# Optimization experiments

Hardware: AMD Instinct MI355X
Metric: run time of the kernel (lower is better)

## Reference

```python
import jax, jax.numpy as jnp
import numpy as np

EMB = 1024
HEADS = 16
HEAD_DIM = EMB // HEADS
FF = 4 * EMB
EPS = 1e-5


def setup_inputs() -> dict:
    key = jax.random.key(0)
    ks = jax.random.split(key, 16)
    s = 0.02
    return {
        "x": jax.random.normal(ks[0], (2, 2048, EMB), dtype=jnp.float32),
        "ln1_g": jnp.ones((EMB,), jnp.float32),
        "ln1_b": jnp.zeros((EMB,), jnp.float32),
        "Wq": jax.random.normal(ks[1], (EMB, EMB), jnp.float32) * s,
        "bq": jnp.zeros((EMB,), jnp.float32),
        "Wk": jax.random.normal(ks[2], (EMB, EMB), jnp.float32) * s,
        "bk": jnp.zeros((EMB,), jnp.float32),
        "Wv": jax.random.normal(ks[3], (EMB, EMB), jnp.float32) * s,
        "bv": jnp.zeros((EMB,), jnp.float32),
        "Wo": jax.random.normal(ks[4], (EMB, EMB), jnp.float32) * s,
        "bo": jnp.zeros((EMB,), jnp.float32),
        "ln2_g": jnp.ones((EMB,), jnp.float32),
        "ln2_b": jnp.zeros((EMB,), jnp.float32),
        "W1": jax.random.normal(ks[5], (EMB, FF), jnp.float32) * s,
        "b1": jnp.zeros((FF,), jnp.float32),
        "W2": jax.random.normal(ks[6], (FF, EMB), jnp.float32) * s,
        "b2": jnp.zeros((EMB,), jnp.float32),
    }


def _layernorm(x, g, b):
    mu = jnp.mean(x, axis=-1, keepdims=True)
    var = jnp.var(x, axis=-1, keepdims=True)
    return (x - mu) * jax.lax.rsqrt(var + EPS) * g + b


def _attention(x, Wq, bq, Wk, bk, Wv, bv, Wo, bo):
    B, T, C = x.shape
    # [B,T,C] -> [B,H,T,Dh]
    def split(y):
        return y.reshape(B, T, HEADS, HEAD_DIM).transpose(0, 2, 1, 3)
    Q = split(x @ Wq + bq)
    K = split(x @ Wk + bk)
    V = split(x @ Wv + bv)
    att = jnp.einsum("bhqd,bhkd->bhqk", Q, K) / np.sqrt(HEAD_DIM).astype(np.float32)
    causal = jnp.tril(jnp.ones((T, T), bool))
    att = jnp.where(causal, att, -jnp.inf)
    att = jax.nn.softmax(att, axis=-1)
    out = jnp.einsum("bhqk,bhkd->bhqd", att, V)
    out = out.transpose(0, 2, 1, 3).reshape(B, T, C)
    return out @ Wo + bo


def reference(x, ln1_g, ln1_b, Wq, bq, Wk, bk, Wv, bv, Wo, bo,
              ln2_g, ln2_b, W1, b1, W2, b2):
    # dropout is identity in eval mode
    x = x + _attention(_layernorm(x, ln1_g, ln1_b), Wq, bq, Wk, bk, Wv, bv, Wo, bo)
    h = _layernorm(x, ln2_g, ln2_b)
    h = jax.nn.gelu(h @ W1 + b1, approximate=False) @ W2 + b2
    return x + h
```

## Files before the change

kernel.cpp:

```cpp
#include <hip/hip_runtime.h>
#include <hip/hip_bf16.h>

typedef __attribute__((ext_vector_type(4))) float f32x4;
typedef __attribute__((ext_vector_type(8))) short bf16x8;
typedef unsigned int u32;
typedef unsigned short u16;

#define GASP __attribute__((address_space(1)))
#define LASP __attribute__((address_space(3)))

__device__ __forceinline__ u16 f2bf(float f) {
  u32 u = __float_as_uint(f);
  return (u16)((u + 0x7fffu + ((u >> 16) & 1u)) >> 16);
}

__device__ __forceinline__ u32 cvtpk(float lo, float hi) {
  u32 r;
  asm("v_cvt_pk_bf16_f32 %0, %1, %2" : "=v"(r) : "v"(lo), "v"(hi));
  return r;
}

__device__ __forceinline__ void gl_lds16(const void* g, void* l) {
  __builtin_amdgcn_global_load_lds((const GASP u32*)g, (LASP u32*)l, 16, 0, 0);
}

struct CastArgs {
  const float* s[6];
  u16* d[6];
};

__global__ __launch_bounds__(256) void cast_w(CastArgs a) {
  int bid = blockIdx.x;
  int w, t, K, N, kshift;
  if (bid < 4096)      { w = bid >> 10; t = bid & 1023; K = 1024; N = 1024; kshift = 5; }
  else if (bid < 8192) { w = 4; t = bid - 4096; K = 1024; N = 4096; kshift = 5; }
  else                 { w = 5; t = bid - 8192; K = 4096; N = 1024; kshift = 7; }
  int tk = t & ((1 << kshift) - 1);
  int tn = t >> kshift;
  int k0 = tk << 5, n0 = tn << 5;
  const float* src = a.s[w];
  u16* dst = a.d[w];
  __shared__ u16 tile[32][36];
  int r = threadIdx.x >> 3, c0 = (threadIdx.x & 7) << 2;
  float4 v = *(const float4*)&src[(size_t)(k0 + r) * N + n0 + c0];
  tile[c0 + 0][r] = f2bf(v.x);
  tile[c0 + 1][r] = f2bf(v.y);
  tile[c0 + 2][r] = f2bf(v.z);
  tile[c0 + 3][r] = f2bf(v.w);
  __syncthreads();
  ushort4 o;
  o.x = tile[r][c0 + 0];
  o.y = tile[r][c0 + 1];
  o.z = tile[r][c0 + 2];
  o.w = tile[r][c0 + 3];
  *(ushort4*)&dst[(size_t)(n0 + r) * K + k0 + c0] = o;
}

__global__ __launch_bounds__(256) void ln_k(const float* __restrict__ x, const float* __restrict__ g,
                                            const float* __restrict__ b, u16* __restrict__ out) {
  int row = blockIdx.x;
  int tid = threadIdx.x;
  float4 v = *(const float4*)&x[(size_t)row * 1024 + tid * 4];
  float s = v.x + v.y + v.z + v.w;
  float ss = v.x * v.x + v.y * v.y + v.z * v.z + v.w * v.w;
#pragma unroll
  for (int o = 32; o >= 1; o >>= 1) {
    s += __shfl_xor(s, o, 64);
    ss += __shfl_xor(ss, o, 64);
  }
  __shared__ float red[8];
  int wv = tid >> 6;
  if ((tid & 63) == 0) { red[wv] = s; red[wv + 4] = ss; }
  __syncthreads();
  s = red[0] + red[1] + red[2] + red[3];
  ss = red[4] + red[5] + red[6] + red[7];
  float mu = s * (1.0f / 1024.0f);
  float var = ss * (1.0f / 1024.0f) - mu * mu;
  float rstd = rsqrtf(var + 1e-5f);
  float4 gv = *(const float4*)&g[tid * 4];
  float4 bv = *(const float4*)&b[tid * 4];
  ushort4 o4;
  o4.x = f2bf((v.x - mu) * rstd * gv.x + bv.x);
  o4.y = f2bf((v.y - mu) * rstd * gv.y + bv.y);
  o4.z = f2bf((v.z - mu) * rstd * gv.z + bv.z);
  o4.w = f2bf((v.w - mu) * rstd * gv.w + bv.w);
  *(ushort4*)&out[(size_t)row * 1024 + tid * 4] = o4;
}

template <int MODE>
__global__ __launch_bounds__(512, 2) void gemm_256(
    const u16* __restrict__ A, const u16* __restrict__ Bt,
    const float* __restrict__ bias0, const float* __restrict__ bias1, const float* __restrict__ bias2,
    void* outp, int rm, int rn, int xn, int M, int N, int K) {
  __shared__ __align__(16) u16 As[4][128 * 64];
  __shared__ __align__(16) u16 Bs[4][128 * 64];
  char* asB = (char*)As;
  char* bsB = (char*)Bs;
  const int tid = threadIdx.x;
  const int w = tid >> 6, lane = tid & 63;
  const int xcd = blockIdx.x & 7, idx = blockIdx.x >> 3;
  const int mt = (xcd / xn) * rm + (idx % rm);
  const int nt = (xcd % xn) * rn + (idx / rm);
  const int m0 = mt << 8, n0 = nt << 8;

  const int rA = tid >> 3;
  const int csw = ((tid & 7) ^ (rA & 7)) * 8;
  const u16* pA = A + (size_t)(m0 + rA) * K + csw;
  const u16* pB = Bt + (size_t)(n0 + rA) * K + csw;
  const int dstOff = tid * 16;

#define STG_A(kt, h, d_) do {                                            \
    const u16* s_ = pA + (size_t)((h) * 128) * K + (size_t)(kt) * 64;    \
    char* l_ = asB + ((d_) * 2 + (h)) * 16384 + dstOff;                  \
    gl_lds16(s_, l_);                                                    \
    gl_lds16(s_ + (size_t)64 * K, l_ + 8192);                            \
  } while (0)
#define STG_B(kt, h, d_) do {                                            \
    const u16* s_ = pB + (size_t)((h) * 128) * K + (size_t)(kt) * 64;    \
    char* l_ = bsB + ((d_) * 2 + (h)) * 16384 + dstOff;                  \
    gl_lds16(s_, l_);                                                    \
    gl_lds16(s_ + (size_t)64 * K, l_ + 8192);                            \
  } while (0)

  const int wr = w >> 2, wc = w & 3;
  const int g = lane >> 4, qi = lane & 15;

  int aOff[8][2], bOff[4][2];
#pragma unroll
  for (int mm = 0; mm < 8; ++mm) {
    int row = mm * 16 + qi;
#pragma unroll
    for (int ks = 0; ks < 2; ++ks)
      aOff[mm][ks] = row * 128 + (((ks * 4 + g) ^ (qi & 7)) << 4);
  }
#pragma unroll
  for (int nn = 0; nn < 4; ++nn) {
    int rowb = (wc & 1) * 64 + nn * 16 + qi;
#pragma unroll
    for (int ks = 0; ks < 2; ++ks)
      bOff[nn][ks] = rowb * 128 + (((ks * 4 + g) ^ (qi & 7)) << 4);
  }

  f32x4 acc[8][4];
#pragma unroll
  for (int i = 0; i < 8; ++i)
#pragma unroll
    for (int j = 0; j < 4; ++j) acc[i][j] = f32x4{0.f, 0.f, 0.f, 0.f};

#define MFMA16(MB, A00, A01, A10, A11) do {                                              \
    __builtin_amdgcn_s_setprio(1);                                                       \
    acc[(MB)][0] = __builtin_amdgcn_mfma_f32_16x16x32_bf16(A00, bv[0][0], acc[(MB)][0], 0, 0, 0); \
    acc[(MB)][1] = __builtin_amdgcn_mfma_f32_16x16x32_bf16(A00, bv[1][0], acc[(MB)][1], 0, 0, 0); \
    acc[(MB)][2] = __builtin_amdgcn_mfma_f32_16x16x32_bf16(A00, bv[2][0], acc[(MB)][2], 0, 0, 0); \
    acc[(MB)][3] = __builtin_amdgcn_mfma_f32_16x16x32_bf16(A00, bv[3][0], acc[(MB)][3], 0, 0, 0); \
    acc[(MB) + 1][0] = __builtin_amdgcn_mfma_f32_16x16x32_bf16(A10, bv[0][0], acc[(MB) + 1][0], 0, 0, 0); \
    acc[(MB) + 1][1] = __builtin_amdgcn_mfma_f32_16x16x32_bf16(A10, bv[1][0], acc[(MB) + 1][1], 0, 0, 0); \
    acc[(MB) + 1][2] = __builtin_amdgcn_mfma_f32_16x16x32_bf16(A10, bv[2][0], acc[(MB) + 1][2], 0, 0, 0); \
    acc[(MB) + 1][3] = __builtin_amdgcn_mfma_f32_16x16x32_bf16(A10, bv[3][0], acc[(MB) + 1][3], 0, 0, 0); \
    acc[(MB)][0] = __builtin_amdgcn_mfma_f32_16x16x32_bf16(A01, bv[0][1], acc[(MB)][0], 0, 0, 0); \
    acc[(MB)][1] = __builtin_amdgcn_mfma_f32_16x16x32_bf16(A01, bv[1][1], acc[(MB)][1], 0, 0, 0); \
    acc[(MB)][2] = __builtin_amdgcn_mfma_f32_16x16x32_bf16(A01, bv[2][1], acc[(MB)][2], 0, 0, 0); \
    acc[(MB)][3] = __builtin_amdgcn_mfma_f32_16x16x32_bf16(A01, bv[3][1], acc[(MB)][3], 0, 0, 0); \
    acc[(MB) + 1][0] = __builtin_amdgcn_mfma_f32_16x16x32_bf16(A11, bv[0][1], acc[(MB) + 1][0], 0, 0, 0); \
    acc[(MB) + 1][1] = __builtin_amdgcn_mfma_f32_16x16x32_bf16(A11, bv[1][1], acc[(MB) + 1][1], 0, 0, 0); \
    acc[(MB) + 1][2] = __builtin_amdgcn_mfma_f32_16x16x32_bf16(A11, bv[2][1], acc[(MB) + 1][2], 0, 0, 0); \
    acc[(MB) + 1][3] = __builtin_amdgcn_mfma_f32_16x16x32_bf16(A11, bv[3][1], acc[(MB) + 1][3], 0, 0, 0); \
    __builtin_amdgcn_s_setprio(0);                                                       \
  } while (0)

#define RDA(dst0, dst1, MB)                                          \
    bf16x8 dst0##0 = *(const bf16x8*)(asB + aTB + aOff[(MB)][0]);     \
    bf16x8 dst0##1 = *(const bf16x8*)(asB + aTB + aOff[(MB)][1]);     \
    bf16x8 dst1##0 = *(const bf16x8*)(asB + aTB + aOff[(MB) + 1][0]); \
    bf16x8 dst1##1 = *(const bf16x8*)(asB + aTB + aOff[(MB) + 1][1]);

  const int T = K >> 6;
  STG_A(0, 0, 0); STG_A(0, 1, 0);
  STG_B(0, 0, 0); STG_B(0, 1, 0);
  asm volatile("s_waitcnt vmcnt(0)" ::: "memory");
  __builtin_amdgcn_s_barrier();

  for (int t = 0; t < T; ++t) {
    const int d = t & 1;
    const int aTB = (d * 2 + wr) * 16384;
    const int bTB = (d * 2 + (wc >> 1)) * 16384;
    bf16x8 bv[4][2];
#pragma unroll
    for (int nn = 0; nn < 4; ++nn) {
      bv[nn][0] = *(const bf16x8*)(bsB + bTB + bOff[nn][0]);
      bv[nn][1] = *(const bf16x8*)(bsB + bTB + bOff[nn][1]);
    }
    RDA(p0a, p0b, 0);
    if (t + 1 < T) STG_A(t + 1, 0, d ^ 1);
    MFMA16(0, p0a0, p0a1, p0b0, p0b1);
    RDA(p1a, p1b, 2);
    if (t + 1 < T) STG_A(t + 1, 1, d ^ 1);
    MFMA16(2, p1a0, p1a1, p1b0, p1b1);
    RDA(p2a, p2b, 4);
    if (t + 1 < T) STG_B(t + 1, 0, d ^ 1);
    MFMA16(4, p2a0, p2a1, p2b0, p2b1);
    RDA(p3a, p3b, 6);
    if (t + 1 < T) STG_B(t + 1, 1, d ^ 1);
    MFMA16(6, p3a0, p3a1, p3b0, p3b1);
    asm volatile("" ::: "memory");
    if (t + 1 < T) { asm volatile("s_waitcnt vmcnt(0)" ::: "memory"); }
    __builtin_amdgcn_s_barrier();
  }
#undef MFMA16
#undef RDA
#undef STG_A
#undef STG_B

  const int ci = lane & 15;
#pragma unroll
  for (int mm = 0; mm < 8; ++mm) {
#pragma unroll
    for (int nn = 0; nn < 4; ++nn) {
      int colb = n0 + wc * 64 + nn * 16 + ci;
      int rowbase = m0 + wr * 128 + mm * 16 + 4 * g;
      f32x4 c = acc[mm][nn];
      if constexpr (MODE == 2) {
        int sel = colb >> 10;
        int cc = colb & 1023;
        const float* bp = sel == 0 ? bias0 : (sel == 1 ? bias1 : bias2);
        float bb = bp[cc];
        int h = cc >> 6, dd = cc & 63;
        int b_ = rowbase >> 11, tt = rowbase & 2047;
        if (sel == 2) {
          u16* op = (u16*)outp + 2ull * (4096ull * 1024ull);
          ushort4 o4;
          o4.x = f2bf(c[0] + bb);
          o4.y = f2bf(c[1] + bb);
          o4.z = f2bf(c[2] + bb);
          o4.w = f2bf(c[3] + bb);
          *(ushort4*)&op[((size_t)(b_ * 16 + h) * 64 + dd) * 2048 + tt] = o4;
        } else {
          float scale = (sel == 0) ? 0.125f : 1.0f;
          u16* op = (u16*)outp + (size_t)sel * (4096ull * 1024ull);
#pragma unroll
          for (int r = 0; r < 4; ++r)
            op[((size_t)(b_ * 16 + h) * 2048 + tt + r) * 64 + dd] = f2bf((c[r] + bb) * scale);
        }
      } else {
        float bb = bias0[colb];
#pragma unroll
        for (int r = 0; r < 4; ++r) {
          float v = c[r] + bb;
          float gl = 0.5f * v * (1.0f + erff(v * 0.70710678118654752f));
          ((u16*)outp)[(size_t)(rowbase + r) * N + colb] = f2bf(gl);
        }
      }
    }
  }
}

__global__ __launch_bounds__(512) void gemm_sk(
    const u16* __restrict__ A, const u16* __restrict__ Bt,
    const float* __restrict__ bias0, float* __restrict__ outp,
    const float* __restrict__ res, int M, int N, int K) {
  __shared__ __align__(16) union SM {
    struct { u16 As[2][4][128 * 32]; u16 Bs[2][4][128 * 32]; } t;
    float red[16][4][4][64];
  } sm;
  const int tid = threadIdx.x;
  const int w8 = tid >> 6, lane = tid & 63;
  const int gg = w8 >> 2, wl = w8 & 3;
  const int m0 = blockIdx.y << 7, n0 = blockIdx.x << 7;

  char* asB = (char*)sm.t.As[gg];
  char* bsB = (char*)sm.t.Bs[gg];
  const u16* aS[2];
  const u16* bS[2];
#pragma unroll
  for (int i = 0; i < 2; ++i) {
    int p = wl * 2048 + i * 1024 + lane * 16;
    int r = p >> 6;
    int cl = ((p >> 4) & 3) ^ ((r >> 1) & 3);
    aS[i] = A + (size_t)(m0 + r) * K + gg * 32 + cl * 8;
    bS[i] = Bt + (size_t)(n0 + r) * K + gg * 32 + cl * 8;
  }
  f32x4 acc[4][4];
#pragma unroll
  for (int i = 0; i < 4; ++i)
#pragma unroll
    for (int j = 0; j < 4; ++j) acc[i][j] = f32x4{0.f, 0.f, 0.f, 0.f};

  const int wr = wl >> 1, wc = wl & 1;
  int aOff[4], bOff[4];
#pragma unroll
  for (int mm = 0; mm < 4; ++mm) {
    int rowa = wr * 64 + mm * 16 + (lane & 15);
    aOff[mm] = rowa * 64 + (((lane >> 4) ^ ((rowa >> 1) & 3)) << 4);
    int rowb = wc * 64 + mm * 16 + (lane & 15);
    bOff[mm] = rowb * 64 + (((lane >> 4) ^ ((rowb >> 1) & 3)) << 4);
  }

  gl_lds16(aS[0], asB + wl * 2048);
  gl_lds16(aS[1], asB + wl * 2048 + 1024);
  gl_lds16(bS[0], bsB + wl * 2048);
  gl_lds16(bS[1], bsB + wl * 2048 + 1024);
  if (K > 64) {
    gl_lds16(aS[0] + 64, asB + 8192 + wl * 2048);
    gl_lds16(aS[1] + 64, asB + 8192 + wl * 2048 + 1024);
    gl_lds16(bS[0] + 64, bsB + 8192 + wl * 2048);
    gl_lds16(bS[1] + 64, bsB + 8192 + wl * 2048 + 1024);
  }
  if (K > 128) {
    gl_lds16(aS[0] + 128, asB + 16384 + wl * 2048);
    gl_lds16(aS[1] + 128, asB + 16384 + wl * 2048 + 1024);
    gl_lds16(bS[0] + 128, bsB + 16384 + wl * 2048);
    gl_lds16(bS[1] + 128, bsB + 16384 + wl * 2048 + 1024);
  }
  int buf = 0;
  for (int ks = 0; ks < K; ks += 64) {
    const int rem = ((K - ks) >> 6) - 1;
    if (rem >= 2)      { asm volatile("s_waitcnt vmcnt(8)" ::: "memory"); }
    else if (rem == 1) { asm volatile("s_waitcnt vmcnt(4)" ::: "memory"); }
    else               { asm volatile("s_waitcnt vmcnt(0)" ::: "memory"); }
    __builtin_amdgcn_s_barrier();
    asm volatile("" ::: "memory");
    if (ks + 192 < K) {
      const int nb = ((buf + 3) & 3) * 8192;
      gl_lds16(aS[0] + ks + 192, asB + nb + wl * 2048);
      gl_lds16(aS[1] + ks + 192, asB + nb + wl * 2048 + 1024);
      gl_lds16(bS[0] + ks + 192, bsB + nb + wl * 2048);
      gl_lds16(bS[1] + ks + 192, bsB + nb + wl * 2048 + 1024);
    }
    const int tb = buf * 8192;
    bf16x8 av[4], bv[4];
#pragma unroll
    for (int mm = 0; mm < 4; ++mm) av[mm] = *(const bf16x8*)(asB + tb + aOff[mm]);
#pragma unroll
    for (int nn = 0; nn < 4; ++nn) bv[nn] = *(const bf16x8*)(bsB + tb + bOff[nn]);
#pragma unroll
    for (int mm = 0; mm < 4; ++mm)
#pragma unroll
      for (int nn = 0; nn < 4; ++nn)
        acc[mm][nn] = __builtin_amdgcn_mfma_f32_16x16x32_bf16(av[mm], bv[nn], acc[mm][nn], 0, 0, 0);
    buf = (buf + 1) & 3;
  }

  __syncthreads();
  if (gg == 1) {
#pragma unroll
    for (int mm = 0; mm < 4; ++mm)
#pragma unroll
      for (int nn = 0; nn < 4; ++nn)
#pragma unroll
        for (int r = 0; r < 4; ++r) sm.red[mm * 4 + nn][r][wl][lane] = acc[mm][nn][r];
  }
  __syncthreads();
  if (gg == 0) {
    const int g = lane >> 4, ci = lane & 15;
#pragma unroll
    for (int mm = 0; mm < 4; ++mm) {
#pragma unroll
      for (int nn = 0; nn < 4; ++nn) {
        int colb = n0 + wc * 64 + nn * 16 + ci;
        int rowbase = m0 + wr * 64 + mm * 16 + 4 * g;
        float bb = bias0[colb];
#pragma unroll
        for (int r = 0; r < 4; ++r) {
          size_t idx = (size_t)(rowbase + r) * N + colb;
          outp[idx] = acc[mm][nn][r] + sm.red[mm * 4 + nn][r][wl][lane] + bb + res[idx];
        }
      }
    }
  }
}

__global__ __launch_bounds__(256, 2) void attn_k(const u16* __restrict__ Q, const u16* __restrict__ Kg,
                                                 const u16* __restrict__ Vt, u16* __restrict__ O) {
  __shared__ __align__(16) u16 Ks[2][64 * 64];
  __shared__ __align__(16) u16 Vs[2][64 * 64];
  const int qt = 15 - (int)blockIdx.y;
  const int bh = blockIdx.x;
  const int tid = threadIdx.x, w = tid >> 6, lane = tid & 63;
  const int g = lane >> 4, qi = lane & 15;
  const u16* Qb = Q + (size_t)bh * 2048 * 64;
  const u16* Kb = Kg + (size_t)bh * 2048 * 64;
  const u16* Vtb = Vt + (size_t)bh * 64 * 2048;

  const int c1 = 256 + tid;
  const int r0 = tid >> 3, r1 = c1 >> 3;
  const int s0 = ((tid & 7) ^ (r0 & 7)) * 8, s1 = ((c1 & 7) ^ (r1 & 7)) * 8;
  const u16* srcK0 = Kb + (size_t)r0 * 64 + s0;
  const u16* srcK1 = Kb + (size_t)r1 * 64 + s1;
  const u16* srcV0 = Vtb + (size_t)r0 * 2048 + s0;
  const u16* srcV1 = Vtb + (size_t)r1 * 2048 + s1;
  char* ksB = (char*)Ks;
  char* vsB = (char*)Vs;
  const int d0 = tid * 16, d1 = c1 * 16;

  int koff[4][2], voff[4][2];
#pragma unroll
  for (int t = 0; t < 4; ++t) {
    int row = 16 * t + qi;
#pragma unroll
    for (int kk = 0; kk < 2; ++kk) {
      koff[t][kk] = row * 128 + (((4 * kk + g) ^ (qi & 7)) << 4);
      voff[t][kk] = koff[t][kk];
    }
  }

  const int b_ = bh >> 4, hh = bh & 15;
  u32* Ou = (u32*)O;

  const int qmin = qt * 128 + w * 32;
  const int qr0 = qmin + qi, qr1 = qmin + 16 + qi;

  bf16x8 qf[2][2];
#pragma unroll
  for (int h = 0; h < 2; ++h)
#pragma unroll
    for (int kk = 0; kk < 2; ++kk)
      qf[h][kk] = *(const bf16x8*)(Qb + (size_t)(qmin + 16 * h + qi) * 64 + kk * 32 + g * 8);

  f32x4 acc0[4], acc1[4];
#pragma unroll
  for (int dt = 0; dt < 4; ++dt) {
    acc0[dt] = f32x4{0.f, 0.f, 0.f, 0.f};
    acc1[dt] = f32x4{0.f, 0.f, 0.f, 0.f};
  }
  float m0 = -1e30f, l0 = 0.0f, m1 = -1e30f, l1 = 0.0f;

  const bool ge = (g & 1) == 0;
  const bool G0 = (g >> 1) == 0;
  const bool innr = (g == 0) || (g == 3);
  union Frag { u32 u[4]; bf16x8 v; };

#define SOFTPACK(ST, ACC, MVAR, LVAR, QROW, F0, F1) do {                      \
    float pvv[4][4];                                                          \
    float tmax = -1e30f;                                                      \
    if (kv0 + 63 > qmin) {                                                    \
      _Pragma("unroll")                                                       \
      for (int t = 0; t < 4; ++t)                                             \
        _Pragma("unroll")                                                     \
        for (int r = 0; r < 4; ++r) {                                         \
          int key = kv0 + 16 * t + 4 * g + r;                                 \
          float sv = ST[t][r];                                                \
          sv = (key <= (QROW)) ? sv : -1e30f;                                 \
          pvv[t][r] = sv;                                                     \
          tmax = fmaxf(tmax, sv);                                             \
        }                                                                     \
    } else {                                                                  \
      _Pragma("unroll")                                                       \
      for (int t = 0; t < 4; ++t)                                             \
        _Pragma("unroll")                                                     \
        for (int r = 0; r < 4; ++r) {                                         \
          float sv = ST[t][r];                                                \
          pvv[t][r] = sv;                                                     \
          tmax = fmaxf(tmax, sv);                                             \
        }                                                                     \
    }                                                                         \
    tmax = fmaxf(tmax, __shfl_xor(tmax, 16, 64));                             \
    tmax = fmaxf(tmax, __shfl_xor(tmax, 32, 64));                             \
    if (!__all(tmax <= MVAR + 8.0f)) {                                        \
      float mn = fmaxf(MVAR, tmax);                                           \
      float corr = __expf(MVAR - mn);                                         \
      LVAR *= corr;                                                           \
      _Pragma("unroll")                                                       \
      for (int dt = 0; dt < 4; ++dt)                                          \
        _Pragma("unroll")                                                     \
        for (int r = 0; r < 4; ++r) ACC[dt][r] *= corr;                       \
      MVAR = mn;                                                              \
    }                                                                         \
    float tsum = 0.f;                                                         \
    _Pragma("unroll")                                                         \
    for (int t = 0; t < 4; ++t)                                               \
      _Pragma("unroll")                                                       \
      for (int r = 0; r < 4; ++r) {                                           \
        float e = __expf(pvv[t][r] - MVAR);                                   \
        pvv[t][r] = e;                                                        \
        tsum += e;                                                            \
      }                                                                       \
    tsum += __shfl_xor(tsum, 16, 64);                                         \
    tsum += __shfl_xor(tsum, 32, 64);                                         \
    LVAR += tsum;                                                             \
    u32 pk[4][2], ex[4][2];                                                   \
    _Pragma("unroll")                                                         \
    for (int t = 0; t < 4; ++t)                                               \
      _Pragma("unroll")                                                       \
      for (int p = 0; p < 2; ++p) {                                           \
        u32 v = cvtpk(pvv[t][2 * p], pvv[t][2 * p + 1]);                      \
        pk[t][p] = v;                                                         \
        ex[t][p] = (u32)__shfl_xor((int)v, 16, 64);                           \
      }                                                                       \
    u32 mm_[4][4];                                                            \
    _Pragma("unroll")                                                         \
    for (int t = 0; t < 4; ++t) {                                             \
      mm_[t][0] = ge ? pk[t][0] : ex[t][0];                                   \
      mm_[t][1] = ge ? pk[t][1] : ex[t][1];                                   \
      mm_[t][2] = ge ? ex[t][0] : pk[t][0];                                   \
      mm_[t][3] = ge ? ex[t][1] : pk[t][1];                                   \
    }                                                                         \
    _Pragma("unroll")                                                         \
    for (int i = 0; i < 4; ++i) {                                             \
      u32 sel0 = G0 ? mm_[1][i] : mm_[0][i];                                  \
      u32 sel1 = G0 ? mm_[3][i] : mm_[2][i];                                  \
      u32 sw0 = (u32)__shfl_xor((int)sel0, 32, 64);                           \
      u32 sw1 = (u32)__shfl_xor((int)sel1, 32, 64);                           \
      u32 own0 = G0 ? mm_[0][i] : mm_[1][i];                                  \
      u32 own1 = G0 ? mm_[2][i] : mm_[3][i];                                  \
      F0.u[i] = innr ? own0 : sw0;                                            \
      F1.u[i] = innr ? own1 : sw1;                                            \
    }                                                                         \
  } while (0)

  gl_lds16(srcK0, ksB + d0);
  gl_lds16(srcK1, ksB + d1);
  gl_lds16(srcV0, vsB + d0);
  gl_lds16(srcV1, vsB + d1);

  const int nsteps = 2 * qt + 2;
  int buf = 0;
  for (int s = 0; s < nsteps; ++s) {
    __syncthreads();
    if (s + 1 < nsteps) {
      int nb = buf ^ 1;
      gl_lds16(srcK0 + (size_t)(s + 1) * 4096, ksB + nb * 8192 + d0);
      gl_lds16(srcK1 + (size_t)(s + 1) * 4096, ksB + nb * 8192 + d1);
      gl_lds16(srcV0 + (size_t)(s + 1) * 64, vsB + nb * 8192 + d0);
      gl_lds16(srcV1 + (size_t)(s + 1) * 64, vsB + nb * 8192 + d1);
    }
    const int kv0 = s * 64;
    if (kv0 <= qmin + 31) {
      const int tb = buf * 8192;
      bf16x8 kf[4][2];
#pragma unroll
      for (int t = 0; t < 4; ++t) {
        kf[t][0] = *(const bf16x8*)(ksB + tb + koff[t][0]);
        kf[t][1] = *(const bf16x8*)(ksB + tb + koff[t][1]);
      }
      f32x4 st0[4], st1[4];
      __builtin_amdgcn_s_setprio(1);
#pragma unroll
      for (int t = 0; t < 4; ++t) {
        st0[t] = f32x4{0.f, 0.f, 0.f, 0.f};
        st0[t] = __builtin_amdgcn_mfma_f32_16x16x32_bf16(kf[t][0], qf[0][0], st0[t], 0, 0, 0);
        st0[t] = __builtin_amdgcn_mfma_f32_16x16x32_bf16(kf[t][1], qf[0][1], st0[t], 0, 0, 0);
      }
#pragma unroll
      for (int t = 0; t < 4; ++t) {
        st1[t] = f32x4{0.f, 0.f, 0.f, 0.f};
        st1[t] = __builtin_amdgcn_mfma_f32_16x16x32_bf16(kf[t][0], qf[1][0], st1[t], 0, 0, 0);
        st1[t] = __builtin_amdgcn_mfma_f32_16x16x32_bf16(kf[t][1], qf[1][1], st1[t], 0, 0, 0);
      }
      __builtin_amdgcn_s_setprio(0);
      bf16x8 vfa[4], vfb[4];
#pragma unroll
      for (int dt = 0; dt < 4; ++dt) {
        vfa[dt] = *(const bf16x8*)(vsB + tb + voff[dt][0]);
        vfb[dt] = *(const bf16x8*)(vsB + tb + voff[dt][1]);
      }
      Frag f00, f10, f01, f11;
      SOFTPACK(st0, acc0, m0, l0, qr0, f00, f10);
      SOFTPACK(st1, acc1, m1, l1, qr1, f01, f11);
      __builtin_amdgcn_s_setprio(1);
#pragma unroll
      for (int dt = 0; dt < 4; ++dt) {
        acc0[dt] = __builtin_amdgcn_mfma_f32_16x16x32_bf16(vfa[dt], f00.v, acc0[dt], 0, 0, 0);
        acc0[dt] = __builtin_amdgcn_mfma_f32_16x16x32_bf16(vfb[dt], f10.v, acc0[dt], 0, 0, 0);
      }
#pragma unroll
      for (int dt = 0; dt < 4; ++dt) {
        acc1[dt] = __builtin_amdgcn_mfma_f32_16x16x32_bf16(vfa[dt], f01.v, acc1[dt], 0, 0, 0);
        acc1[dt] = __builtin_amdgcn_mfma_f32_16x16x32_bf16(vfb[dt], f11.v, acc1[dt], 0, 0, 0);
      }
      __builtin_amdgcn_s_setprio(0);
    }
    buf ^= 1;
  }
#undef SOFTPACK

  {
    float rl = 1.0f / l0;
    size_t rowq = (size_t)(b_ * 2048 + qr0);
#pragma unroll
    for (int dt = 0; dt < 4; ++dt) {
#pragma unroll
      for (int rp = 0; rp < 2; ++rp) {
        u16 lo = f2bf(acc0[dt][rp * 2] * rl);
        u16 hi = f2bf(acc0[dt][rp * 2 + 1] * rl);
        u32 pkd = (u32)lo | ((u32)hi << 16);
        size_t off = rowq * 1024 + hh * 64 + dt * 16 + 4 * g + rp * 2;
        Ou[off >> 1] = pkd;
      }
    }
  }
  {
    float rl = 1.0f / l1;
    size_t rowq = (size_t)(b_ * 2048 + qr1);
#pragma unroll
    for (int dt = 0; dt < 4; ++dt) {
#pragma unroll
      for (int rp = 0; rp < 2; ++rp) {
        u16 lo = f2bf(acc1[dt][rp * 2] * rl);
        u16 hi = f2bf(acc1[dt][rp * 2 + 1] * rl);
        u32 pkd = (u32)lo | ((u32)hi << 16);
        size_t off = rowq * 1024 + hh * 64 + dt * 16 + 4 * g + rp * 2;
        Ou[off >> 1] = pkd;
      }
    }
  }
}

extern "C" void kernel_launch(void* const* d_in, const int* in_sizes, int n_in,
                              void* d_out, int out_size, void* d_ws, size_t ws_size,
                              hipStream_t stream) {
  const float* x    = (const float*)d_in[0];
  const float* ln1g = (const float*)d_in[1];
  const float* ln1b = (const float*)d_in[2];
  const float* Wq   = (const float*)d_in[3];
  const float* bq   = (const float*)d_in[4];
  const float* Wk   = (const float*)d_in[5];
  const float* bk   = (const float*)d_in[6];
  const float* Wv   = (const float*)d_in[7];
  const float* bv   = (const float*)d_in[8];
  const float* Wo   = (const float*)d_in[9];
  const float* bo   = (const float*)d_in[10];
  const float* ln2g = (const float*)d_in[11];
  const float* ln2b = (const float*)d_in[12];
  const float* W1   = (const float*)d_in[13];
  const float* b1   = (const float*)d_in[14];
  const float* W2   = (const float*)d_in[15];
  const float* b2   = (const float*)d_in[16];

  char* ws = (char*)d_ws;
  const size_t MB = 1ull << 20;
  u16* WqT = (u16*)(ws + 0 * MB);
  u16* WkT = (u16*)(ws + 2 * MB);
  u16* WvT = (u16*)(ws + 4 * MB);
  u16* WoT = (u16*)(ws + 6 * MB);
  u16* W1T = (u16*)(ws + 8 * MB);
  u16* W2T = (u16*)(ws + 16 * MB);
  u16* XN  = (u16*)(ws + 24 * MB);
  u16* Qb  = (u16*)(ws + 32 * MB);
  u16* Kb  = (u16*)(ws + 40 * MB);
  u16* Vtb = (u16*)(ws + 48 * MB);
  u16* Ob  = (u16*)(ws + 56 * MB);
  u16* Gb  = (u16*)(ws + 32 * MB);

  CastArgs ca;
  ca.s[0] = Wq; ca.s[1] = Wk; ca.s[2] = Wv; ca.s[3] = Wo; ca.s[4] = W1; ca.s[5] = W2;
  ca.d[0] = WqT; ca.d[1] = WkT; ca.d[2] = WvT; ca.d[3] = WoT; ca.d[4] = W1T; ca.d[5] = W2T;
  cast_w<<<12288, 256, 0, stream>>>(ca);

  ln_k<<<4096, 256, 0, stream>>>(x, ln1g, ln1b, XN);

  gemm_256<2><<<192, 512, 0, stream>>>(XN, WqT, bq, bk, bv, Qb, 4, 6, 2, 4096, 3072, 1024);

  attn_k<<<dim3(32, 16), 256, 0, stream>>>(Qb, Kb, Vtb, Ob);

  gemm_sk<<<dim3(8, 32), 512, 0, stream>>>(Ob, WoT, bo, (float*)d_out, x, 4096, 1024, 1024);

  ln_k<<<4096, 256, 0, stream>>>((const float*)d_out, ln2g, ln2b, XN);

  gemm_256<3><<<256, 512, 0, stream>>>(XN, W1T, b1, nullptr, nullptr, Gb, 8, 4, 4, 4096, 4096, 1024);

  gemm_sk<<<dim3(8, 32), 512, 0, stream>>>(Gb, W2T, b2, (float*)d_out, (const float*)d_out, 4096, 1024, 4096);
}
```

Before: 246.2 us.

## Double attention query tile to 256 rows with 512-thread blocks

The attention kernel now runs 8 waves per block, each covering 32 query rows, so a block handles 256 queries instead of 128. Each K/V tile loaded into LDS is reused by twice as many query rows, and each thread issues one async load per tile instead of two. The grid halves to 256 blocks and the reversed tile ordering (heaviest causal tiles first) is dropped. This risks worse load balance across causal tiles, fewer blocks to fill the GPU, and more waves in a block idling on masked steps while still waiting at the barriers.

Measured after the change: 255.1 us. +3.7%, slower.

```diff
diff --git a/kernel.cpp b/kernel.cpp
--- a/kernel.cpp
+++ b/kernel.cpp
@@ -369,11 +369,11 @@
   }
 }
 
-__global__ __launch_bounds__(256, 2) void attn_k(const u16* __restrict__ Q, const u16* __restrict__ Kg,
-                                                 const u16* __restrict__ Vt, u16* __restrict__ O) {
+__global__ __launch_bounds__(512) void attn_k(const u16* __restrict__ Q, const u16* __restrict__ Kg,
+                                              const u16* __restrict__ Vt, u16* __restrict__ O) {
   __shared__ __align__(16) u16 Ks[2][64 * 64];
   __shared__ __align__(16) u16 Vs[2][64 * 64];
-  const int qt = 15 - (int)blockIdx.y;
+  const int qt = blockIdx.y;
   const int bh = blockIdx.x;
   const int tid = threadIdx.x, w = tid >> 6, lane = tid & 63;
   const int g = lane >> 4, qi = lane & 15;
@@ -381,32 +381,27 @@
   const u16* Kb = Kg + (size_t)bh * 2048 * 64;
   const u16* Vtb = Vt + (size_t)bh * 64 * 2048;
 
-  const int c1 = 256 + tid;
-  const int r0 = tid >> 3, r1 = c1 >> 3;
-  const int s0 = ((tid & 7) ^ (r0 & 7)) * 8, s1 = ((c1 & 7) ^ (r1 & 7)) * 8;
-  const u16* srcK0 = Kb + (size_t)r0 * 64 + s0;
-  const u16* srcK1 = Kb + (size_t)r1 * 64 + s1;
-  const u16* srcV0 = Vtb + (size_t)r0 * 2048 + s0;
-  const u16* srcV1 = Vtb + (size_t)r1 * 2048 + s1;
+  const int rS = tid >> 3, cS = tid & 7;
+  const int csw = (cS ^ (rS & 7)) * 8;
+  const u16* srcK = Kb + (size_t)rS * 64 + csw;
+  const u16* srcV = Vtb + (size_t)rS * 2048 + csw;
   char* ksB = (char*)Ks;
   char* vsB = (char*)Vs;
-  const int d0 = tid * 16, d1 = c1 * 16;
-
-  int koff[4][2], voff[4][2];
+  const int dstOff = tid * 16;
+
+  int koff[4][2];
 #pragma unroll
   for (int t = 0; t < 4; ++t) {
     int row = 16 * t + qi;
 #pragma unroll
-    for (int kk = 0; kk < 2; ++kk) {
+    for (int kk = 0; kk < 2; ++kk)
       koff[t][kk] = row * 128 + (((4 * kk + g) ^ (qi & 7)) << 4);
-      voff[t][kk] = koff[t][kk];
-    }
   }
 
   const int b_ = bh >> 4, hh = bh & 15;
   u32* Ou = (u32*)O;
 
-  const int qmin = qt * 128 + w * 32;
+  const int qmin = qt * 256 + w * 32;
   const int qr0 = qmin + qi, qr1 = qmin + 16 + qi;
 
   bf16x8 qf[2][2];
@@ -507,21 +502,17 @@
     }                                                                         \
   } while (0)
 
-  gl_lds16(srcK0, ksB + d0);
-  gl_lds16(srcK1, ksB + d1);
-  gl_lds16(srcV0, vsB + d0);
-  gl_lds16(srcV1, vsB + d1);
-
-  const int nsteps = 2 * qt + 2;
+  gl_lds16(srcK, ksB + dstOff);
+  gl_lds16(srcV, vsB + dstOff);
+
+  const int nsteps = 4 * (qt + 1);
   int buf = 0;
   for (int s = 0; s < nsteps; ++s) {
     __syncthreads();
     if (s + 1 < nsteps) {
       int nb = buf ^ 1;
-      gl_lds16(srcK0 + (size_t)(s + 1) * 4096, ksB + nb * 8192 + d0);
-      gl_lds16(srcK1 + (size_t)(s + 1) * 4096, ksB + nb * 8192 + d1);
-      gl_lds16(srcV0 + (size_t)(s + 1) * 64, vsB + nb * 8192 + d0);
-      gl_lds16(srcV1 + (size_t)(s + 1) * 64, vsB + nb * 8192 + d1);
+      gl_lds16(srcK + (size_t)(s + 1) * 4096, ksB + nb * 8192 + dstOff);
+      gl_lds16(srcV + (size_t)(s + 1) * 64, vsB + nb * 8192 + dstOff);
     }
     const int kv0 = s * 64;
     if (kv0 <= qmin + 31) {
@@ -550,8 +541,8 @@
       bf16x8 vfa[4], vfb[4];
 #pragma unroll
       for (int dt = 0; dt < 4; ++dt) {
-        vfa[dt] = *(const bf16x8*)(vsB + tb + voff[dt][0]);
-        vfb[dt] = *(const bf16x8*)(vsB + tb + voff[dt][1]);
+        vfa[dt] = *(const bf16x8*)(vsB + tb + koff[dt][0]);
+        vfb[dt] = *(const bf16x8*)(vsB + tb + koff[dt][1]);
       }
       Frag f00, f10, f01, f11;
       SOFTPACK(st0, acc0, m0, l0, qr0, f00, f10);
@@ -650,7 +641,7 @@
 
   gemm_256<2><<<192, 512, 0, stream>>>(XN, WqT, bq, bk, bv, Qb, 4, 6, 2, 4096, 3072, 1024);
 
-  attn_k<<<dim3(32, 16), 256, 0, stream>>>(Qb, Kb, Vtb, Ob);
+  attn_k<<<dim3(32, 8), 512, 0, stream>>>(Qb, Kb, Vtb, Ob);
 
   gemm_sk<<<dim3(8, 32), 512, 0, stream>>>(Ob, WoT, bo, (float*)d_out, x, 4096, 1024, 1024);
 
```
